# Kernel optimization log

Measured on AMD Instinct MI355X. Metric: run time of the kernel, lower is better.

The kernel has to match this reference:

```python
import jax, jax.numpy as jnp
import numpy as np

N, INC, INN, OUTC, OUTN, MAXD = 8, 64, 20000, 64, 8000, 32


def setup_inputs() -> dict:
    key = jax.random.key(0)
    k0, k1, k2, k3, k4 = jax.random.split(key, 5)
    # adjacency list: outn nodes, degree in [8, 32], padded to MAXD with index 0
    rng = np.random.default_rng(0)
    deg = rng.integers(8, MAXD + 1, size=OUTN)                      # (outn,)
    A_np = rng.integers(0, INN, size=(OUTN, MAXD))                  # (outn, maxD)
    valid = np.arange(MAXD)[None, :] < deg[:, None]
    A_np = np.where(valid, A_np, 0)
    # '_norm' option: mask entries are 1/degree for valid slots, 0 for pad
    mask_np = valid.astype(np.float32) / deg[:, None].astype(np.float32)

    x = jax.random.normal(k0, (N, INC, INN), dtype=jnp.float32)
    # hadamard weight: sqrt(2/inn) * U(-1, 1)
    weight = np.sqrt(2.0 / INN).astype(np.float32) * (
        2.0 * jax.random.uniform(k1, (INC, INN), dtype=jnp.float32) - 1.0)
    # weight_norm Linear(inc, outc): v (outc, inc) direction, g (outc,) magnitude
    ct_v = jax.random.normal(k2, (OUTC, INC), dtype=jnp.float32) * (1.0 / np.sqrt(INC).astype(np.float32))
    ct_g = 0.5 + jax.random.uniform(k3, (OUTC,), dtype=jnp.float32)
    bias = 0.2 * jax.random.normal(k4, (1, OUTC, OUTN), dtype=jnp.float32)
    return {
        'x': x,
        'weight': weight,
        'ct_v': ct_v,
        'ct_g': ct_g,
        'bias': bias,
        'mask': jnp.asarray(mask_np),
        'A': jnp.asarray(A_np, dtype=jnp.int32),
    }


def reference(x, weight, ct_v, ct_g, bias, mask, A):
    # x: (N, inc, inn); weight: (inc, inn)
    xw = x * weight                                   # hadamard
    gathered = xw[:, :, A]                            # (N, inc, outn, maxD) adjacency gather
    pooled = jnp.einsum('bcod,od->bco', gathered, mask)  # degree-normalized masked sum
    # weight_norm: W = g * v / ||v||_row
    W = ct_g[:, None] * ct_v / jnp.linalg.norm(ct_v, axis=1, keepdims=True)  # (outc, inc)
    y = jnp.einsum('bco,kc->bko', pooled, W)          # (N, outc, outn)
    return y + bias
```

## Files before the change

kernel.cpp:

```cpp
#include <hip/hip_runtime.h>
#include <stdint.h>

#define NB   8
#define INC  64
#define INN  20000
#define OUTC 64
#define OUTN 8000
#define MAXD 32
#define NG   16

__device__ __forceinline__ uint32_t pack_bf16_2(float a, float b) {
    uint32_t ua = __float_as_uint(a);
    uint32_t ub = __float_as_uint(b);
    uint32_t ra = (ua + 0x7FFFu + ((ua >> 16) & 1u)) >> 16;
    uint32_t rb = (ub + 0x7FFFu + ((ub >> 16) & 1u)) >> 16;
    return (ra & 0xFFFFu) | (rb << 16);
}

__global__ void prep_kernel(const int* __restrict__ A, const float* __restrict__ mask,
                            const float* __restrict__ ct_v, const float* __restrict__ ct_g,
                            uint4* __restrict__ AQ, float2* __restrict__ scale2,
                            float* __restrict__ W_T) {
    if (blockIdx.x == 64) {
        int k = threadIdx.x;
        if (k < OUTC) {
            float s = 0.f;
            for (int c = 0; c < INC; ++c) { float v = ct_v[k * INC + c]; s += v * v; }
            float inv = ct_g[k] / sqrtf(s);
            for (int c = 0; c < INC; ++c) W_T[c * OUTC + k] = ct_v[k * INC + c] * inv;
        }
        return;
    }
    int o = blockIdx.x * 128 + threadIdx.x;
    if (o >= OUTN) return;
    const int4* arow = (const int4*)(A + (size_t)o * MAXD);
#pragma unroll
    for (int j = 0; j < 4; ++j) {
        int4 v0 = arow[2 * j];
        int4 v1 = arow[2 * j + 1];
        uint4 pk;
        pk.x = (uint32_t)(v0.x << 1) | ((uint32_t)(v0.y << 1) << 16);
        pk.y = (uint32_t)(v0.z << 1) | ((uint32_t)(v0.w << 1) << 16);
        pk.z = (uint32_t)(v1.x << 1) | ((uint32_t)(v1.y << 1) << 16);
        pk.w = (uint32_t)(v1.z << 1) | ((uint32_t)(v1.w << 1) << 16);
        AQ[(size_t)j * OUTN + o] = pk;
    }
    float invdeg = mask[(size_t)o * MAXD];
    float deg    = rintf(1.0f / invdeg);
    scale2[o] = make_float2(invdeg, 32.0f - deg);
}

__global__ __launch_bounds__(256)
void xw_kernel(const float* __restrict__ x, const float* __restrict__ w,
               uint2* __restrict__ xwi) {
    int t    = threadIdx.x;
    int tile = blockIdx.x;
    int g    = blockIdx.y;
    int b    = blockIdx.z;
    int i0   = tile * 1024 + t * 4;
    if (i0 >= INN) return;
    float4 p[4];
#pragma unroll
    for (int cl = 0; cl < 4; ++cl) {
        int c = g * 4 + cl;
        float4 xv = *(const float4*)(x + ((size_t)(b * INC + c)) * INN + i0);
        float4 wv = *(const float4*)(w + (size_t)c * INN + i0);
        p[cl] = make_float4(xv.x * wv.x, xv.y * wv.y, xv.z * wv.z, xv.w * wv.w);
    }
    uint4 o01, o23;
    o01.x = pack_bf16_2(p[0].x, p[1].x);  o01.y = pack_bf16_2(p[2].x, p[3].x);
    o01.z = pack_bf16_2(p[0].y, p[1].y);  o01.w = pack_bf16_2(p[2].y, p[3].y);
    o23.x = pack_bf16_2(p[0].z, p[1].z);  o23.y = pack_bf16_2(p[2].z, p[3].z);
    o23.z = pack_bf16_2(p[0].w, p[1].w);  o23.w = pack_bf16_2(p[2].w, p[3].w);
    uint2* dst = xwi + ((size_t)(b * NG + g)) * INN + i0;
    ((uint4*)dst)[0] = o01;
    ((uint4*)dst)[1] = o23;
}

__global__ __launch_bounds__(1024, 4)
void gather_kernel(const uint2* __restrict__ xwi, const uint4* __restrict__ AQ,
                   const float2* __restrict__ scale2, float* __restrict__ pooled) {
    __shared__ __align__(16) uint2 smem[INN];
    int h = blockIdx.x;
    int g = blockIdx.y;
    int b = blockIdx.z;
    int tid = threadIdx.x;
    int c0 = g * 4;

    const uint4* src = (const uint4*)(xwi + ((size_t)(b * NG + g)) * INN);
#pragma unroll
    for (int k = 0; k < 10; ++k) {
        int i = tid + k * 1024;
        if (i < INN / 2) {
            __builtin_amdgcn_global_load_lds(
                (const __attribute__((address_space(1))) uint32_t*)(src + i),
                (__attribute__((address_space(3))) uint32_t*)((char*)smem + ((i & ~63) * 16)),
                16, 0, 0);
        }
    }

    int obase = h * (OUTN / 2);
    int oend  = obase + (OUTN / 2);
    int o0 = obase + tid;
    uint4 q0 = AQ[o0];
    uint4 q1 = AQ[OUTN + o0];
    uint4 q2 = AQ[2 * OUTN + o0];
    uint4 q3 = AQ[3 * OUTN + o0];

    __syncthreads();

    uint2 z = smem[0];
    float z0 = __uint_as_float(z.x << 16);
    float z1 = __uint_as_float(z.x & 0xFFFF0000u);
    float z2 = __uint_as_float(z.y << 16);
    float z3 = __uint_as_float(z.y & 0xFFFF0000u);

    const char* sb = (const char*)smem;

#pragma unroll
    for (int it = 0; it < 4; ++it) {
        int o = obase + tid + it * 1024;
        uint4 n0 = q0, n1 = q1, n2 = q2, n3 = q3;
        if (it < 3) {
            int op = o + 1024; if (op >= oend) op = oend - 1;
            n0 = AQ[op];
            n1 = AQ[OUTN + op];
            n2 = AQ[2 * OUTN + op];
            n3 = AQ[3 * OUTN + op];
        }
        if (o < oend) {
            float a0 = 0.f, a1 = 0.f, a2 = 0.f, a3 = 0.f;
#define DO_U32(u)                                                      \
            {                                                          \
                uint32_t off0 = (u & 0xFFFFu) << 2;                    \
                uint32_t off1 = (u >> 16) << 2;                        \
                uint2 v0 = *(const uint2*)(sb + off0);                 \
                uint2 v1 = *(const uint2*)(sb + off1);                 \
                a0 += __uint_as_float(v0.x << 16);                     \
                a1 += __uint_as_float(v0.x & 0xFFFF0000u);             \
                a2 += __uint_as_float(v0.y << 16);                     \
                a3 += __uint_as_float(v0.y & 0xFFFF0000u);             \
                a0 += __uint_as_float(v1.x << 16);                     \
                a1 += __uint_as_float(v1.x & 0xFFFF0000u);             \
                a2 += __uint_as_float(v1.y << 16);                     \
                a3 += __uint_as_float(v1.y & 0xFFFF0000u);             \
            }
            DO_U32(q0.x) DO_U32(q0.y) DO_U32(q0.z) DO_U32(q0.w)
            DO_U32(q1.x) DO_U32(q1.y) DO_U32(q1.z) DO_U32(q1.w)
            DO_U32(q2.x) DO_U32(q2.y) DO_U32(q2.z) DO_U32(q2.w)
            DO_U32(q3.x) DO_U32(q3.y) DO_U32(q3.z) DO_U32(q3.w)
#undef DO_U32
            float2 sc = scale2[o];
            a0 = (a0 - sc.y * z0) * sc.x;
            a1 = (a1 - sc.y * z1) * sc.x;
            a2 = (a2 - sc.y * z2) * sc.x;
            a3 = (a3 - sc.y * z3) * sc.x;
            pooled[((size_t)(b * OUTC + c0 + 0)) * OUTN + o] = a0;
            pooled[((size_t)(b * OUTC + c0 + 1)) * OUTN + o] = a1;
            pooled[((size_t)(b * OUTC + c0 + 2)) * OUTN + o] = a2;
            pooled[((size_t)(b * OUTC + c0 + 3)) * OUTN + o] = a3;
        }
        q0 = n0; q1 = n1; q2 = n2; q3 = n3;
    }
}

__global__ __launch_bounds__(256)
void out_kernel(float* io, const float* __restrict__ W_T,
                const float* __restrict__ bias) {
    __shared__ __align__(16) float sp[INC][128];
    __shared__ __align__(16) float sw[INC][OUTC];
    int obase = blockIdx.x * 128;
    int b     = blockIdx.y;

    const float* pb = io + (size_t)b * INC * OUTN;
    for (int idx = threadIdx.x; idx < INC * 32; idx += 256) {
        int c  = idx >> 5;
        int q  = idx & 31;
        int o4 = obase + q * 4;
        float4 v = (o4 < OUTN) ? *(const float4*)(pb + (size_t)c * OUTN + o4)
                               : make_float4(0.f, 0.f, 0.f, 0.f);
        *(float4*)(&sp[c][q * 4]) = v;
    }
    for (int idx = threadIdx.x; idx < (INC * OUTC) / 4; idx += 256) {
        ((float4*)sw)[idx] = ((const float4*)W_T)[idx];
    }
    __syncthreads();

    int t   = threadIdx.x;
    int kt  = t >> 4;
    int ot0 = (t & 15) * 8;
    int k0  = kt * 4;

    float acc[4][8];
#pragma unroll
    for (int kk = 0; kk < 4; ++kk) {
#pragma unroll
        for (int jh = 0; jh < 2; ++jh) {
            int o4 = obase + ot0 + jh * 4;
            float4 bv = (o4 < OUTN)
                ? *(const float4*)(bias + (size_t)(k0 + kk) * OUTN + o4)
                : make_float4(0.f, 0.f, 0.f, 0.f);
            acc[kk][jh * 4 + 0] = bv.x;
            acc[kk][jh * 4 + 1] = bv.y;
            acc[kk][jh * 4 + 2] = bv.z;
            acc[kk][jh * 4 + 3] = bv.w;
        }
    }

#pragma unroll 4
    for (int c = 0; c < INC; ++c) {
        float4 w4  = *(const float4*)(&sw[c][k0]);
        float4 pa  = *(const float4*)(&sp[c][ot0]);
        float4 pb4 = *(const float4*)(&sp[c][ot0 + 4]);
        float p[8] = {pa.x, pa.y, pa.z, pa.w, pb4.x, pb4.y, pb4.z, pb4.w};
        float wv[4] = {w4.x, w4.y, w4.z, w4.w};
#pragma unroll
        for (int kk = 0; kk < 4; ++kk)
#pragma unroll
            for (int j = 0; j < 8; ++j)
                acc[kk][j] += wv[kk] * p[j];
    }

    int o0 = obase + ot0;
    if (o0 < OUTN) {
#pragma unroll
        for (int kk = 0; kk < 4; ++kk) {
            float4 s0 = make_float4(acc[kk][0], acc[kk][1], acc[kk][2], acc[kk][3]);
            float4 s1 = make_float4(acc[kk][4], acc[kk][5], acc[kk][6], acc[kk][7]);
            float* dst = io + ((size_t)(b * OUTC + k0 + kk)) * OUTN + o0;
            *(float4*)(dst)     = s0;
            *(float4*)(dst + 4) = s1;
        }
    }
}

extern "C" void kernel_launch(void* const* d_in, const int* in_sizes, int n_in,
                              void* d_out, int out_size, void* d_ws, size_t ws_size,
                              hipStream_t stream) {
    const float* x    = (const float*)d_in[0];
    const float* w    = (const float*)d_in[1];
    const float* ct_v = (const float*)d_in[2];
    const float* ct_g = (const float*)d_in[3];
    const float* bias = (const float*)d_in[4];
    const float* mask = (const float*)d_in[5];
    const int*   A    = (const int*)d_in[6];
    float* y = (float*)d_out;

    char* ws = (char*)d_ws;
    uint2*  xwi    = (uint2*)(ws);
    uint4*  AQ     = (uint4*)(ws + 20480000);
    float2* scale2 = (float2*)(ws + 20992000);
    float*  W_T    = (float*)(ws + 21056000);

    xw_kernel<<<dim3(20, NG, NB), 256, 0, stream>>>(x, w, xwi);
    prep_kernel<<<65, 128, 0, stream>>>(A, mask, ct_v, ct_g, AQ, scale2, W_T);
    gather_kernel<<<dim3(2, NG, NB), 1024, 0, stream>>>(xwi, AQ, scale2, y);
    out_kernel<<<dim3(63, NB), 256, 0, stream>>>(y, W_T, bias);
}
```

Baseline: 51.05 us.

## Store hadamard intermediate as scaled fp8 and pool 8 channels per block

Replaces the bf16 intermediate with fp8 (pre-scaled by 256 to keep small values representable), halving the intermediate buffer. Each gather block now handles 8 channels per LDS staging and a quarter of the output nodes, so each index decode serves twice as many channels. The goal is to cut intermediate memory traffic and gather work per channel. The cost is a large loss of precision, with e4m3 accumulated over up to 32 terms, which may break tolerance.

Result: faster. 49.13 us (-3.8%).

```diff
diff --git a/kernel.cpp b/kernel.cpp
--- a/kernel.cpp
+++ b/kernel.cpp
@@ -7,15 +7,8 @@
 #define OUTC 64
 #define OUTN 8000
 #define MAXD 32
-#define NG   16
-
-__device__ __forceinline__ uint32_t pack_bf16_2(float a, float b) {
-    uint32_t ua = __float_as_uint(a);
-    uint32_t ub = __float_as_uint(b);
-    uint32_t ra = (ua + 0x7FFFu + ((ua >> 16) & 1u)) >> 16;
-    uint32_t rb = (ub + 0x7FFFu + ((ub >> 16) & 1u)) >> 16;
-    return (ra & 0xFFFFu) | (rb << 16);
-}
+
+typedef float f32x2 __attribute__((ext_vector_type(2)));
 
 __global__ void prep_kernel(const int* __restrict__ A, const float* __restrict__ mask,
                             const float* __restrict__ ct_v, const float* __restrict__ ct_g,
@@ -47,7 +40,7 @@
     }
     float invdeg = mask[(size_t)o * MAXD];
     float deg    = rintf(1.0f / invdeg);
-    scale2[o] = make_float2(invdeg, 32.0f - deg);
+    scale2[o] = make_float2(invdeg * (1.0f / 256.0f), 32.0f - deg);
 }
 
 __global__ __launch_bounds__(256)
@@ -55,39 +48,45 @@
                uint2* __restrict__ xwi) {
     int t    = threadIdx.x;
     int tile = blockIdx.x;
-    int g    = blockIdx.y;
+    int g8   = blockIdx.y;
     int b    = blockIdx.z;
-    int i0   = tile * 1024 + t * 4;
+    int i0   = (tile * 256 + t) * 2;
     if (i0 >= INN) return;
-    float4 p[4];
-#pragma unroll
-    for (int cl = 0; cl < 4; ++cl) {
-        int c = g * 4 + cl;
-        float4 xv = *(const float4*)(x + ((size_t)(b * INC + c)) * INN + i0);
-        float4 wv = *(const float4*)(w + (size_t)c * INN + i0);
-        p[cl] = make_float4(xv.x * wv.x, xv.y * wv.y, xv.z * wv.z, xv.w * wv.w);
-    }
-    uint4 o01, o23;
-    o01.x = pack_bf16_2(p[0].x, p[1].x);  o01.y = pack_bf16_2(p[2].x, p[3].x);
-    o01.z = pack_bf16_2(p[0].y, p[1].y);  o01.w = pack_bf16_2(p[2].y, p[3].y);
-    o23.x = pack_bf16_2(p[0].z, p[1].z);  o23.y = pack_bf16_2(p[2].z, p[3].z);
-    o23.z = pack_bf16_2(p[0].w, p[1].w);  o23.w = pack_bf16_2(p[2].w, p[3].w);
-    uint2* dst = xwi + ((size_t)(b * NG + g)) * INN + i0;
-    ((uint4*)dst)[0] = o01;
-    ((uint4*)dst)[1] = o23;
+    int c0 = g8 * 8;
+    const float* xb = x + ((size_t)b * INC + c0) * INN + i0;
+    const float* wb = w + (size_t)c0 * INN + i0;
+    float p0[8], p1[8];
+#pragma unroll
+    for (int cl = 0; cl < 8; ++cl) {
+        float2 xv = *(const float2*)(xb + (size_t)cl * INN);
+        float2 wv = *(const float2*)(wb + (size_t)cl * INN);
+        p0[cl] = xv.x * wv.x * 256.0f;
+        p1[cl] = xv.y * wv.y * 256.0f;
+    }
+    uint32_t a0, a1, b0, b1;
+    a0 = __builtin_amdgcn_cvt_pk_fp8_f32(p0[0], p0[1], 0,  false);
+    a0 = __builtin_amdgcn_cvt_pk_fp8_f32(p0[2], p0[3], a0, true);
+    a1 = __builtin_amdgcn_cvt_pk_fp8_f32(p0[4], p0[5], 0,  false);
+    a1 = __builtin_amdgcn_cvt_pk_fp8_f32(p0[6], p0[7], a1, true);
+    b0 = __builtin_amdgcn_cvt_pk_fp8_f32(p1[0], p1[1], 0,  false);
+    b0 = __builtin_amdgcn_cvt_pk_fp8_f32(p1[2], p1[3], b0, true);
+    b1 = __builtin_amdgcn_cvt_pk_fp8_f32(p1[4], p1[5], 0,  false);
+    b1 = __builtin_amdgcn_cvt_pk_fp8_f32(p1[6], p1[7], b1, true);
+    uint4 out = make_uint4(a0, a1, b0, b1);
+    *(uint4*)(xwi + ((size_t)(b * 8 + g8)) * INN + i0) = out;
 }
 
 __global__ __launch_bounds__(1024, 4)
 void gather_kernel(const uint2* __restrict__ xwi, const uint4* __restrict__ AQ,
                    const float2* __restrict__ scale2, float* __restrict__ pooled) {
     __shared__ __align__(16) uint2 smem[INN];
-    int h = blockIdx.x;
-    int g = blockIdx.y;
-    int b = blockIdx.z;
+    int s  = blockIdx.x;
+    int g8 = blockIdx.y;
+    int b  = blockIdx.z;
     int tid = threadIdx.x;
-    int c0 = g * 4;
-
-    const uint4* src = (const uint4*)(xwi + ((size_t)(b * NG + g)) * INN);
+    int c0 = g8 * 8;
+
+    const uint4* src = (const uint4*)(xwi + ((size_t)(b * 8 + g8)) * INN);
 #pragma unroll
     for (int k = 0; k < 10; ++k) {
         int i = tid + k * 1024;
@@ -99,8 +98,8 @@
         }
     }
 
-    int obase = h * (OUTN / 2);
-    int oend  = obase + (OUTN / 2);
+    int obase = s * (OUTN / 4);
+    int oend  = obase + (OUTN / 4);
     int o0 = obase + tid;
     uint4 q0 = AQ[o0];
     uint4 q1 = AQ[OUTN + o0];
@@ -109,19 +108,20 @@
 
     __syncthreads();
 
-    uint2 z = smem[0];
-    float z0 = __uint_as_float(z.x << 16);
-    float z1 = __uint_as_float(z.x & 0xFFFF0000u);
-    float z2 = __uint_as_float(z.y << 16);
-    float z3 = __uint_as_float(z.y & 0xFFFF0000u);
+    uint2 zw = smem[0];
+    f32x2 ze0 = __builtin_amdgcn_cvt_pk_f32_fp8(zw.x, false);
+    f32x2 ze1 = __builtin_amdgcn_cvt_pk_f32_fp8(zw.x, true);
+    f32x2 ze2 = __builtin_amdgcn_cvt_pk_f32_fp8(zw.y, false);
+    f32x2 ze3 = __builtin_amdgcn_cvt_pk_f32_fp8(zw.y, true);
+    float z[8] = {ze0.x, ze0.y, ze1.x, ze1.y, ze2.x, ze2.y, ze3.x, ze3.y};
 
     const char* sb = (const char*)smem;
 
 #pragma unroll
-    for (int it = 0; it < 4; ++it) {
+    for (int it = 0; it < 2; ++it) {
         int o = obase + tid + it * 1024;
         uint4 n0 = q0, n1 = q1, n2 = q2, n3 = q3;
-        if (it < 3) {
+        if (it == 0) {
             int op = o + 1024; if (op >= oend) op = oend - 1;
             n0 = AQ[op];
             n1 = AQ[OUTN + op];
@@ -129,21 +129,30 @@
             n3 = AQ[3 * OUTN + op];
         }
         if (o < oend) {
-            float a0 = 0.f, a1 = 0.f, a2 = 0.f, a3 = 0.f;
-#define DO_U32(u)                                                      \
-            {                                                          \
-                uint32_t off0 = (u & 0xFFFFu) << 2;                    \
-                uint32_t off1 = (u >> 16) << 2;                        \
-                uint2 v0 = *(const uint2*)(sb + off0);                 \
-                uint2 v1 = *(const uint2*)(sb + off1);                 \
-                a0 += __uint_as_float(v0.x << 16);                     \
-                a1 += __uint_as_float(v0.x & 0xFFFF0000u);             \
-                a2 += __uint_as_float(v0.y << 16);                     \
-                a3 += __uint_as_float(v0.y & 0xFFFF0000u);             \
-                a0 += __uint_as_float(v1.x << 16);                     \
-                a1 += __uint_as_float(v1.x & 0xFFFF0000u);             \
-                a2 += __uint_as_float(v1.y << 16);                     \
-                a3 += __uint_as_float(v1.y & 0xFFFF0000u);             \
+            float a[8] = {0.f, 0.f, 0.f, 0.f, 0.f, 0.f, 0.f, 0.f};
+#define DO_U32(u)                                                       \
+            {                                                           \
+                uint32_t off0 = (u & 0xFFFFu) << 2;                     \
+                uint32_t off1 = (u >> 16) << 2;                         \
+                uint2 v0 = *(const uint2*)(sb + off0);                  \
+                uint2 v1 = *(const uint2*)(sb + off1);                  \
+                f32x2 e;                                                \
+                e = __builtin_amdgcn_cvt_pk_f32_fp8(v0.x, false);       \
+                a[0] += e.x; a[1] += e.y;                               \
+                e = __builtin_amdgcn_cvt_pk_f32_fp8(v0.x, true);        \
+                a[2] += e.x; a[3] += e.y;                               \
+                e = __builtin_amdgcn_cvt_pk_f32_fp8(v0.y, false);       \
+                a[4] += e.x; a[5] += e.y;                               \
+                e = __builtin_amdgcn_cvt_pk_f32_fp8(v0.y, true);        \
+                a[6] += e.x; a[7] += e.y;                               \
+                e = __builtin_amdgcn_cvt_pk_f32_fp8(v1.x, false);       \
+                a[0] += e.x; a[1] += e.y;                               \
+                e = __builtin_amdgcn_cvt_pk_f32_fp8(v1.x, true);        \
+                a[2] += e.x; a[3] += e.y;                               \
+                e = __builtin_amdgcn_cvt_pk_f32_fp8(v1.y, false);       \
+                a[4] += e.x; a[5] += e.y;                               \
+                e = __builtin_amdgcn_cvt_pk_f32_fp8(v1.y, true);        \
+                a[6] += e.x; a[7] += e.y;                               \
             }
             DO_U32(q0.x) DO_U32(q0.y) DO_U32(q0.z) DO_U32(q0.w)
             DO_U32(q1.x) DO_U32(q1.y) DO_U32(q1.z) DO_U32(q1.w)
@@ -151,14 +160,11 @@
             DO_U32(q3.x) DO_U32(q3.y) DO_U32(q3.z) DO_U32(q3.w)
 #undef DO_U32
             float2 sc = scale2[o];
-            a0 = (a0 - sc.y * z0) * sc.x;
-            a1 = (a1 - sc.y * z1) * sc.x;
-            a2 = (a2 - sc.y * z2) * sc.x;
-            a3 = (a3 - sc.y * z3) * sc.x;
-            pooled[((size_t)(b * OUTC + c0 + 0)) * OUTN + o] = a0;
-            pooled[((size_t)(b * OUTC + c0 + 1)) * OUTN + o] = a1;
-            pooled[((size_t)(b * OUTC + c0 + 2)) * OUTN + o] = a2;
-            pooled[((size_t)(b * OUTC + c0 + 3)) * OUTN + o] = a3;
+#pragma unroll
+            for (int cl = 0; cl < 8; ++cl) {
+                float r = (a[cl] - sc.y * z[cl]) * sc.x;
+                pooled[((size_t)(b * OUTC + c0 + cl)) * OUTN + o] = r;
+            }
         }
         q0 = n0; q1 = n1; q2 = n2; q3 = n3;
     }
@@ -248,12 +254,12 @@
 
     char* ws = (char*)d_ws;
     uint2*  xwi    = (uint2*)(ws);
-    uint4*  AQ     = (uint4*)(ws + 20480000);
-    float2* scale2 = (float2*)(ws + 20992000);
-    float*  W_T    = (float*)(ws + 21056000);
-
-    xw_kernel<<<dim3(20, NG, NB), 256, 0, stream>>>(x, w, xwi);
+    uint4*  AQ     = (uint4*)(ws + 10240000);
+    float2* scale2 = (float2*)(ws + 10752000);
+    float*  W_T    = (float*)(ws + 10816000);
+
+    xw_kernel<<<dim3(40, 8, NB), 256, 0, stream>>>(x, w, xwi);
     prep_kernel<<<65, 128, 0, stream>>>(A, mask, ct_v, ct_g, AQ, scale2, W_T);
-    gather_kernel<<<dim3(2, NG, NB), 1024, 0, stream>>>(xwi, AQ, scale2, y);
+    gather_kernel<<<dim3(4, 8, NB), 1024, 0, stream>>>(xwi, AQ, scale2, y);
     out_kernel<<<dim3(63, NB), 256, 0, stream>>>(y, W_T, bias);
 }
```

## Store hadamard product as scaled FP8 and split gather across more blocks

Applied to the files above, without the earlier changes.

The intermediate x*weight tensor is now stored as FP8 (scaled by 256, with the scale folded into the per-node normalization) instead of BF16. This halves the intermediate buffer and the per-block shared-memory staging, so more blocks fit per CU. The gather grid goes from 2 to 8 output slices per (batch, group), one node per thread, with no inner prefetch loop. The cost is much lower precision in the pooled sums, which risks exceeding the accuracy tolerance.

New measurement: 52.57 us. 1.03x slower.

```diff
diff --git a/kernel.cpp b/kernel.cpp
--- a/kernel.cpp
+++ b/kernel.cpp
@@ -7,15 +7,8 @@
 #define OUTC 64
 #define OUTN 8000
 #define MAXD 32
-#define NG   16
-
-__device__ __forceinline__ uint32_t pack_bf16_2(float a, float b) {
-    uint32_t ua = __float_as_uint(a);
-    uint32_t ub = __float_as_uint(b);
-    uint32_t ra = (ua + 0x7FFFu + ((ua >> 16) & 1u)) >> 16;
-    uint32_t rb = (ub + 0x7FFFu + ((ub >> 16) & 1u)) >> 16;
-    return (ra & 0xFFFFu) | (rb << 16);
-}
+
+typedef float f32x2 __attribute__((ext_vector_type(2)));
 
 __global__ void prep_kernel(const int* __restrict__ A, const float* __restrict__ mask,
                             const float* __restrict__ ct_v, const float* __restrict__ ct_g,
@@ -47,51 +40,63 @@
     }
     float invdeg = mask[(size_t)o * MAXD];
     float deg    = rintf(1.0f / invdeg);
-    scale2[o] = make_float2(invdeg, 32.0f - deg);
+    scale2[o] = make_float2(invdeg * (1.0f / 256.0f), 32.0f - deg);
 }
 
 __global__ __launch_bounds__(256)
 void xw_kernel(const float* __restrict__ x, const float* __restrict__ w,
-               uint2* __restrict__ xwi) {
+               uint32_t* __restrict__ xwi) {
     int t    = threadIdx.x;
     int tile = blockIdx.x;
     int g    = blockIdx.y;
     int b    = blockIdx.z;
     int i0   = tile * 1024 + t * 4;
     if (i0 >= INN) return;
+    int c0 = g * 4;
+    const float* xb = x + ((size_t)b * INC + c0) * INN + i0;
+    const float* wb = w + (size_t)c0 * INN + i0;
     float4 p[4];
 #pragma unroll
     for (int cl = 0; cl < 4; ++cl) {
-        int c = g * 4 + cl;
-        float4 xv = *(const float4*)(x + ((size_t)(b * INC + c)) * INN + i0);
-        float4 wv = *(const float4*)(w + (size_t)c * INN + i0);
-        p[cl] = make_float4(xv.x * wv.x, xv.y * wv.y, xv.z * wv.z, xv.w * wv.w);
-    }
-    uint4 o01, o23;
-    o01.x = pack_bf16_2(p[0].x, p[1].x);  o01.y = pack_bf16_2(p[2].x, p[3].x);
-    o01.z = pack_bf16_2(p[0].y, p[1].y);  o01.w = pack_bf16_2(p[2].y, p[3].y);
-    o23.x = pack_bf16_2(p[0].z, p[1].z);  o23.y = pack_bf16_2(p[2].z, p[3].z);
-    o23.z = pack_bf16_2(p[0].w, p[1].w);  o23.w = pack_bf16_2(p[2].w, p[3].w);
-    uint2* dst = xwi + ((size_t)(b * NG + g)) * INN + i0;
-    ((uint4*)dst)[0] = o01;
-    ((uint4*)dst)[1] = o23;
-}
-
-__global__ __launch_bounds__(1024, 4)
-void gather_kernel(const uint2* __restrict__ xwi, const uint4* __restrict__ AQ,
+        float4 xv = *(const float4*)(xb + (size_t)cl * INN);
+        float4 wv = *(const float4*)(wb + (size_t)cl * INN);
+        p[cl] = make_float4(xv.x * wv.x * 256.0f, xv.y * wv.y * 256.0f,
+                            xv.z * wv.z * 256.0f, xv.w * wv.w * 256.0f);
+    }
+    uint4 out;
+    {
+        uint32_t u;
+        u = __builtin_amdgcn_cvt_pk_fp8_f32(p[0].x, p[1].x, 0, false);
+        u = __builtin_amdgcn_cvt_pk_fp8_f32(p[2].x, p[3].x, u, true);
+        out.x = u;
+        u = __builtin_amdgcn_cvt_pk_fp8_f32(p[0].y, p[1].y, 0, false);
+        u = __builtin_amdgcn_cvt_pk_fp8_f32(p[2].y, p[3].y, u, true);
+        out.y = u;
+        u = __builtin_amdgcn_cvt_pk_fp8_f32(p[0].z, p[1].z, 0, false);
+        u = __builtin_amdgcn_cvt_pk_fp8_f32(p[2].z, p[3].z, u, true);
+        out.z = u;
+        u = __builtin_amdgcn_cvt_pk_fp8_f32(p[0].w, p[1].w, 0, false);
+        u = __builtin_amdgcn_cvt_pk_fp8_f32(p[2].w, p[3].w, u, true);
+        out.w = u;
+    }
+    *(uint4*)(xwi + ((size_t)(b * 16 + g)) * INN + i0) = out;
+}
+
+__global__ __launch_bounds__(1024, 8)
+void gather_kernel(const uint32_t* __restrict__ xwi, const uint4* __restrict__ AQ,
                    const float2* __restrict__ scale2, float* __restrict__ pooled) {
-    __shared__ __align__(16) uint2 smem[INN];
-    int h = blockIdx.x;
-    int g = blockIdx.y;
-    int b = blockIdx.z;
+    __shared__ __align__(16) uint32_t smem[INN];
+    int s  = blockIdx.x;
+    int g  = blockIdx.y;
+    int b  = blockIdx.z;
     int tid = threadIdx.x;
     int c0 = g * 4;
 
-    const uint4* src = (const uint4*)(xwi + ((size_t)(b * NG + g)) * INN);
-#pragma unroll
-    for (int k = 0; k < 10; ++k) {
+    const uint4* src = (const uint4*)(xwi + ((size_t)(b * 16 + g)) * INN);
+#pragma unroll
+    for (int k = 0; k < 5; ++k) {
         int i = tid + k * 1024;
-        if (i < INN / 2) {
+        if (i < INN / 4) {
             __builtin_amdgcn_global_load_lds(
                 (const __attribute__((address_space(1))) uint32_t*)(src + i),
                 (__attribute__((address_space(3))) uint32_t*)((char*)smem + ((i & ~63) * 16)),
@@ -99,68 +104,55 @@
         }
     }
 
-    int obase = h * (OUTN / 2);
-    int oend  = obase + (OUTN / 2);
-    int o0 = obase + tid;
-    uint4 q0 = AQ[o0];
-    uint4 q1 = AQ[OUTN + o0];
-    uint4 q2 = AQ[2 * OUTN + o0];
-    uint4 q3 = AQ[3 * OUTN + o0];
+    int obase = s * 1000;
+    int o     = obase + tid;
+    int oc    = (tid < 1000) ? o : obase;
+    uint4 q0 = AQ[oc];
+    uint4 q1 = AQ[OUTN + oc];
+    uint4 q2 = AQ[2 * OUTN + oc];
+    uint4 q3 = AQ[3 * OUTN + oc];
+    float2 sc = scale2[oc];
 
     __syncthreads();
 
-    uint2 z = smem[0];
-    float z0 = __uint_as_float(z.x << 16);
-    float z1 = __uint_as_float(z.x & 0xFFFF0000u);
-    float z2 = __uint_as_float(z.y << 16);
-    float z3 = __uint_as_float(z.y & 0xFFFF0000u);
+    uint32_t zw = smem[0];
+    f32x2 ze0 = __builtin_amdgcn_cvt_pk_f32_fp8(zw, false);
+    f32x2 ze1 = __builtin_amdgcn_cvt_pk_f32_fp8(zw, true);
 
     const char* sb = (const char*)smem;
-
-#pragma unroll
-    for (int it = 0; it < 4; ++it) {
-        int o = obase + tid + it * 1024;
-        uint4 n0 = q0, n1 = q1, n2 = q2, n3 = q3;
-        if (it < 3) {
-            int op = o + 1024; if (op >= oend) op = oend - 1;
-            n0 = AQ[op];
-            n1 = AQ[OUTN + op];
-            n2 = AQ[2 * OUTN + op];
-            n3 = AQ[3 * OUTN + op];
-        }
-        if (o < oend) {
-            float a0 = 0.f, a1 = 0.f, a2 = 0.f, a3 = 0.f;
-#define DO_U32(u)                                                      \
-            {                                                          \
-                uint32_t off0 = (u & 0xFFFFu) << 2;                    \
-                uint32_t off1 = (u >> 16) << 2;                        \
-                uint2 v0 = *(const uint2*)(sb + off0);                 \
-                uint2 v1 = *(const uint2*)(sb + off1);                 \
-                a0 += __uint_as_float(v0.x << 16);                     \
-                a1 += __uint_as_float(v0.x & 0xFFFF0000u);             \
-                a2 += __uint_as_float(v0.y << 16);                     \
-                a3 += __uint_as_float(v0.y & 0xFFFF0000u);             \
-                a0 += __uint_as_float(v1.x << 16);                     \
-                a1 += __uint_as_float(v1.x & 0xFFFF0000u);             \
-                a2 += __uint_as_float(v1.y << 16);                     \
-                a3 += __uint_as_float(v1.y & 0xFFFF0000u);             \
-            }
-            DO_U32(q0.x) DO_U32(q0.y) DO_U32(q0.z) DO_U32(q0.w)
-            DO_U32(q1.x) DO_U32(q1.y) DO_U32(q1.z) DO_U32(q1.w)
-            DO_U32(q2.x) DO_U32(q2.y) DO_U32(q2.z) DO_U32(q2.w)
-            DO_U32(q3.x) DO_U32(q3.y) DO_U32(q3.z) DO_U32(q3.w)
+    float a0 = 0.f, a1 = 0.f, a2 = 0.f, a3 = 0.f;
+
+#define DO_U32(u)                                                   \
+    {                                                               \
+        uint32_t off0 = (u & 0xFFFFu) << 1;                         \
+        uint32_t off1 = (u >> 16) << 1;                             \
+        uint32_t v0 = *(const uint32_t*)(sb + off0);                \
+        uint32_t v1 = *(const uint32_t*)(sb + off1);                \
+        f32x2 e;                                                    \
+        e = __builtin_amdgcn_cvt_pk_f32_fp8(v0, false);             \
+        a0 += e.x; a1 += e.y;                                       \
+        e = __builtin_amdgcn_cvt_pk_f32_fp8(v0, true);              \
+        a2 += e.x; a3 += e.y;                                       \
+        e = __builtin_amdgcn_cvt_pk_f32_fp8(v1, false);             \
+        a0 += e.x; a1 += e.y;                                       \
+        e = __builtin_amdgcn_cvt_pk_f32_fp8(v1, true);              \
+        a2 += e.x; a3 += e.y;                                       \
+    }
+    DO_U32(q0.x) DO_U32(q0.y) DO_U32(q0.z) DO_U32(q0.w)
+    DO_U32(q1.x) DO_U32(q1.y) DO_U32(q1.z) DO_U32(q1.w)
+    DO_U32(q2.x) DO_U32(q2.y) DO_U32(q2.z) DO_U32(q2.w)
+    DO_U32(q3.x) DO_U32(q3.y) DO_U32(q3.z) DO_U32(q3.w)
 #undef DO_U32
-            float2 sc = scale2[o];
-            a0 = (a0 - sc.y * z0) * sc.x;
-            a1 = (a1 - sc.y * z1) * sc.x;
-            a2 = (a2 - sc.y * z2) * sc.x;
-            a3 = (a3 - sc.y * z3) * sc.x;
-            pooled[((size_t)(b * OUTC + c0 + 0)) * OUTN + o] = a0;
-            pooled[((size_t)(b * OUTC + c0 + 1)) * OUTN + o] = a1;
-            pooled[((size_t)(b * OUTC + c0 + 2)) * OUTN + o] = a2;
-            pooled[((size_t)(b * OUTC + c0 + 3)) * OUTN + o] = a3;
-        }
-        q0 = n0; q1 = n1; q2 = n2; q3 = n3;
+
+    if (tid < 1000) {
+        float r0 = (a0 - sc.y * ze0.x) * sc.x;
+        float r1 = (a1 - sc.y * ze0.y) * sc.x;
+        float r2 = (a2 - sc.y * ze1.x) * sc.x;
+        float r3 = (a3 - sc.y * ze1.y) * sc.x;
+        pooled[((size_t)(b * OUTC + c0 + 0)) * OUTN + o] = r0;
+        pooled[((size_t)(b * OUTC + c0 + 1)) * OUTN + o] = r1;
+        pooled[((size_t)(b * OUTC + c0 + 2)) * OUTN + o] = r2;
+        pooled[((size_t)(b * OUTC + c0 + 3)) * OUTN + o] = r3;
     }
 }
 
@@ -247,13 +239,13 @@
     float* y = (float*)d_out;
 
     char* ws = (char*)d_ws;
-    uint2*  xwi    = (uint2*)(ws);
-    uint4*  AQ     = (uint4*)(ws + 20480000);
-    float2* scale2 = (float2*)(ws + 20992000);
-    float*  W_T    = (float*)(ws + 21056000);
-
-    xw_kernel<<<dim3(20, NG, NB), 256, 0, stream>>>(x, w, xwi);
+    uint32_t* xwi    = (uint32_t*)(ws);
+    uint4*    AQ     = (uint4*)(ws + 10240000);
+    float2*   scale2 = (float2*)(ws + 10752000);
+    float*    W_T    = (float*)(ws + 10816000);
+
+    xw_kernel<<<dim3(20, 16, NB), 256, 0, stream>>>(x, w, xwi);
     prep_kernel<<<65, 128, 0, stream>>>(A, mask, ct_v, ct_g, AQ, scale2, W_T);
-    gather_kernel<<<dim3(2, NG, NB), 1024, 0, stream>>>(xwi, AQ, scale2, y);
+    gather_kernel<<<dim3(8, 16, NB), 1024, 0, stream>>>(xwi, AQ, scale2, y);
     out_kernel<<<dim3(63, NB), 256, 0, stream>>>(y, W_T, bias);
 }
```
